# Performance work log

Measured on AMD Instinct MI355X. Metric: run time of the kernel, lower is better.

The kernel has to match this reference:

```python
import jax, jax.numpy as jnp
import numpy as np

SCALE, K, PATCH, STRIDE = 2, 5, 3, 1
EPS = 1e-5


def im2patch(x, p, s):
    # x: (b,c,H,W) -> (b,c,p,p,m1,m2), 'VALID' patches (padding is 0 for our sizes)
    b, c, H, W = x.shape
    m1 = (H - p) // s + 1
    m2 = (W - p) // s + 1
    ii = (jnp.arange(m1) * s)[:, None] + jnp.arange(p)[None, :]   # (m1,p)
    jj = (jnp.arange(m2) * s)[:, None] + jnp.arange(p)[None, :]   # (m2,p)
    pt = x[:, :, ii[:, :, None, None], jj[None, None, :, :]]      # (b,c,m1,p,m2,p)
    return pt.transpose(0, 1, 3, 5, 2, 4)                         # (b,c,p,p,m1,m2)


def patch2im(patches, p, s):
    # overlap-add fold, averaged by per-pixel patch counts (torch F.fold / ones-fold divisor)
    b, c, _, _, m1, m2 = patches.shape
    Hp = (m1 - 1) * s + p
    Wp = (m2 - 1) * s + p
    out = jnp.zeros((b, c, Hp, Wp), patches.dtype)
    cnt = jnp.zeros((Hp, Wp), patches.dtype)
    for i in range(p):          # fixed small loop over patch offsets (p*p = 36)
        for j in range(p):
            out = out.at[:, :, i:i + s * m1:s, j:j + s * m2:s].add(patches[:, :, i, j])
            cnt = cnt.at[i:i + s * m1:s, j:j + s * m2:s].add(1.0)
    return out / cnt


def setup_inputs():
    key = jax.random.key(0)
    k1, k2, k3 = jax.random.split(key, 3)
    b, cy, H, W = 1, 64, 80, 80
    y = jax.random.normal(k1, (b, cy, H, W), jnp.float32)
    yd = jax.random.normal(k2, (b, cy * SCALE ** 2, H // SCALE, W // SCALE), jnp.float32)
    m = ((H - PATCH) // STRIDE + 1) ** 2
    n = ((H // SCALE - PATCH) // STRIDE + 1) ** 2
    idx_k = jax.random.randint(k3, (b, m, K), 0, n, jnp.int32)
    return {"y": y, "yd": yd, "idx_k": idx_k}


def reference(y, yd, idx_k):
    b, cy, H, W = y.shape
    c = yd.shape[1]           # = cy * scale^2
    rs = SCALE ** 2
    y_p = im2patch(y, PATCH, STRIDE)      # (b,cy,p,p,m1,m2)
    yd_p = im2patch(yd, PATCH, STRIDE)    # (b,c,p,p,n1,n2)
    m1, m2 = y_p.shape[-2:]
    n1, n2 = yd_p.shape[-2:]
    m, n = m1 * m2, n1 * n2
    f = c * PATCH * PATCH
    y_flat = y_p.transpose(0, 4, 5, 1, 2, 3).reshape(b, m, f // rs)
    yd_flat = yd_p.transpose(0, 4, 5, 1, 2, 3).reshape(b, n, f)
    # top-k neighbor gather: (b,n,f)[idx (b,m,k)] -> (b,m,k,f) -> (b,m,f,k)
    z = jax.vmap(lambda t, i: t[i])(yd_flat, idx_k)
    z = z.transpose(0, 1, 3, 2)
    # AdaIN: normalize gathered HR patches, apply LR query patch stats (unbiased var, torch default)
    y_n = y_flat.reshape(b, m, c // rs, PATCH * PATCH)
    z_n = z.reshape(b, m, c // rs, rs * PATCH * PATCH, K)
    z_mu = z_n.mean(axis=3, keepdims=True)
    z_sd = jnp.sqrt(z_n.var(axis=3, ddof=1, keepdims=True) + EPS)
    y_mu = y_n.mean(axis=3, keepdims=True)[..., None]        # (b,m,c',1,1)
    y_sd = jnp.sqrt(y_n.var(axis=3, ddof=1, keepdims=True) + EPS)[..., None]
    z = ((z_n - z_mu) / z_sd * y_sd + y_mu).reshape(b, m, f, K)
    # rearrange f = (cy, scale, scale, p1, p2) into SR patches (b, k*cy, p*scale, p*scale, m1, m2)
    z = z.transpose(0, 3, 2, 1)                                   # (b,k,f,m)
    z = z.reshape(b, K, cy, SCALE, SCALE, PATCH, PATCH, m1, m2)
    z = z.transpose(0, 1, 2, 5, 3, 6, 4, 7, 8)                    # (b,k,cy,p1,s,p2,s,m1,m2)
    z = z.reshape(b, K * cy, PATCH * SCALE, PATCH * SCALE, m1, m2)
    z_sr = patch2im(z, PATCH * SCALE, STRIDE * SCALE)             # (b,k*cy,H*scale,W*scale)
    return z_sr.reshape(b, K * cy, H * SCALE, W * SCALE)
```

## Files before the change

kernel.cpp:

```cpp
#include <hip/hip_runtime.h>

#define CY     64
#define HY     80
#define HD     40
#define SPD    (HD*HD)
#define M1     78
#define N1     38
#define M_TOT  (M1*M1)
#define N_TOT  (N1*N1)
#define KK     5
#define HS     160
#define EPSF   1e-5f
#define LP     33

__device__ __forceinline__ unsigned bf16pk(float a, float b) {
    unsigned ua = __float_as_uint(a), ub = __float_as_uint(b);
    ua = (ua + 0x7fffu + ((ua >> 16) & 1u)) >> 16;
    ub = (ub + 0x7fffu + ((ub >> 16) & 1u)) >> 16;
    return ua | (ub << 16);
}

__global__ __launch_bounds__(256) void pre_kernel(const float* __restrict__ y,
                                                  const float* __restrict__ yd,
                                                  uint2* __restrict__ ydT4h,
                                                  float2* __restrict__ zstT,
                                                  float2* __restrict__ ystT) {
    int id = blockIdx.x * 256 + threadIdx.x;
    if (id < SPD * 64) {
        int cc = id & 63, sp = id >> 6;
        float v0 = yd[(cc * 4 + 0) * SPD + sp];
        float v1 = yd[(cc * 4 + 1) * SPD + sp];
        float v2 = yd[(cc * 4 + 2) * SPD + sp];
        float v3 = yd[(cc * 4 + 3) * SPD + sp];
        ydT4h[sp * 64 + cc] = make_uint2(bf16pk(v0, v1), bf16pk(v2, v3));
        return;
    }
    id -= SPD * 64;
    if (id < N_TOT * 64) {
        int n  = id % N_TOT;
        int cc = id / N_TOT;
        int ni = n / N1, nj = n - ni * N1;
        const float* base = yd + (cc * 4) * SPD + ni * HD + nj;
        float s = 0.f, sq = 0.f;
#pragma unroll
        for (int r = 0; r < 4; ++r)
#pragma unroll
            for (int i = 0; i < 3; ++i)
#pragma unroll
                for (int j = 0; j < 3; ++j) {
                    float v = base[r * SPD + i * HD + j];
                    s += v; sq += v * v;
                }
        float mu  = s * (1.f / 36.f);
        float var = (sq - 36.f * mu * mu) * (1.f / 35.f);
        zstT[n * 64 + cc] = make_float2(mu, rsqrtf(var + EPSF));
        return;
    }
    id -= N_TOT * 64;
    if (id >= CY * M_TOT) return;
    int m  = id % M_TOT;
    int cc = id / M_TOT;
    int mi = m / M1, mj = m - mi * M1;
    const float* base = y + cc * (HY * HY) + mi * HY + mj;
    float s = 0.f, sq = 0.f;
#pragma unroll
    for (int i = 0; i < 3; ++i)
#pragma unroll
        for (int j = 0; j < 3; ++j) {
            float v = base[i * HY + j];
            s += v; sq += v * v;
        }
    float mu  = s * (1.f / 9.f);
    float var = (sq - 9.f * mu * mu) * (1.f / 8.f);
    ystT[m * 64 + cc] = make_float2(mu, sqrtf(var + EPSF));
}

__global__ __launch_bounds__(256) void coef_kernel(const int* __restrict__ idx,
                                                   const float2* __restrict__ zstT,
                                                   const float2* __restrict__ ystT,
                                                   unsigned* __restrict__ coef,
                                                   int* __restrict__ nsp) {
    int gid = blockIdx.x * 256 + threadIdx.x;
    int cc = gid & 63;
    int pair = gid >> 6;
    int k = pair / M_TOT, m = pair - k * M_TOT;
    int n = __builtin_amdgcn_readfirstlane(idx[m * KK + k]);
    float2 ys = ystT[m * 64 + cc];
    float2 zs = zstT[n * 64 + cc];
    float a = ys.y * zs.y;
    float b = fmaf(-zs.x, a, ys.x);
    coef[(size_t)pair * 64 + cc] = bf16pk(a, b);
    if (cc == 0) nsp[pair] = (n / N1) * HD + (n - (n / N1) * N1);
}

__device__ __forceinline__ float bflo(unsigned u) { return __uint_as_float(u << 16); }
__device__ __forceinline__ float bfhi(unsigned u) { return __uint_as_float(u & 0xffff0000u); }

__global__ __launch_bounds__(512) void agg_kernel(
    const uint2* __restrict__ ydT4h, const unsigned* __restrict__ coef,
    const int* __restrict__ nsp, float* __restrict__ out)
{
    __shared__ float lds[128 * LP];

    int lane = threadIdx.x & 63;
    int w    = __builtin_amdgcn_readfirstlane(threadIdx.x >> 6);
    int bid  = blockIdx.x;
    int wg   = (bid & 7) * 250 + (bid >> 3);
    int k    = wg / 400;
    int rem  = wg - k * 400;
    int y    = rem / 5;
    int xb2  = rem - y * 5;
    int x0   = xb2 * 16 + w * 2;

    const unsigned* cfk  = coef + (size_t)k * M_TOT * 64;
    const int*      nspk = nsp + k * M_TOT;

    float acc[2][4];
    float bs[2] = {0.f, 0.f};
    float inv[2];
#pragma unroll
    for (int q = 0; q < 2; ++q)
#pragma unroll
        for (int r = 0; r < 4; ++r) acc[q][r] = 0.f;

    if (y >= 2 && y <= M1 - 1 && x0 >= 2 && x0 <= M1 - 2) {
        inv[0] = inv[1] = 1.f / 9.f;
        int      spv[12];
        unsigned cf[12];
#pragma unroll
        for (int p = 0; p < 12; ++p) {
            int m = (y - 2 + (p >> 2)) * M1 + (x0 - 2 + (p & 3));
            spv[p] = nspk[m];
            cf[p]  = cfk[m * 64 + lane];
        }
        int spb[12];
#pragma unroll
        for (int p = 0; p < 12; ++p)
            spb[p] = __builtin_amdgcn_readfirstlane(spv[p]);
#pragma unroll
        for (int r = 0; r < 3; ++r) {
            int b0 = spb[r * 4 + 0] + (2 - r) * HD;
            int b1 = spb[r * 4 + 1] + (2 - r) * HD;
            int b2 = spb[r * 4 + 2] + (2 - r) * HD;
            int b3 = spb[r * 4 + 3] + (2 - r) * HD;
            uint2 vA0 = ydT4h[(b0 + 2) * 64 + lane];
            uint2 vA1 = ydT4h[(b1 + 1) * 64 + lane];
            uint2 vA2 = ydT4h[(b2 + 0) * 64 + lane];
            uint2 vB0 = ydT4h[(b1 + 2) * 64 + lane];
            uint2 vB1 = ydT4h[(b2 + 1) * 64 + lane];
            uint2 vB2 = ydT4h[(b3 + 0) * 64 + lane];
            uint2 vA[3] = {vA0, vA1, vA2};
            uint2 vB[3] = {vB0, vB1, vB2};
#pragma unroll
            for (int c = 0; c < 3; ++c) {
                {
                    unsigned cv = cf[r * 4 + c];
                    float a = bfhi(cv) , dummy;
                    (void)dummy;
                    float aa = bflo(cv), bb = bfhi(cv);
                    bs[0] += bb;
                    acc[0][0] = fmaf(aa, bflo(vA[c].x), acc[0][0]);
                    acc[0][1] = fmaf(aa, bfhi(vA[c].x), acc[0][1]);
                    acc[0][2] = fmaf(aa, bflo(vA[c].y), acc[0][2]);
                    acc[0][3] = fmaf(aa, bfhi(vA[c].y), acc[0][3]);
                    (void)a;
                }
                {
                    unsigned cv = cf[r * 4 + c + 1];
                    float aa = bflo(cv), bb = bfhi(cv);
                    bs[1] += bb;
                    acc[1][0] = fmaf(aa, bflo(vB[c].x), acc[1][0]);
                    acc[1][1] = fmaf(aa, bfhi(vB[c].x), acc[1][1]);
                    acc[1][2] = fmaf(aa, bflo(vB[c].y), acc[1][2]);
                    acc[1][3] = fmaf(aa, bfhi(vB[c].y), acc[1][3]);
                }
            }
        }
    } else {
#pragma unroll
        for (int q = 0; q < 2; ++q) {
            int x = x0 + q;
            int milo = max(0, y - 2), mihi = min(M1 - 1, y);
            int mjlo = max(0, x - 2), mjhi = min(M1 - 1, x);
            inv[q] = 1.f / (float)((mihi - milo + 1) * (mjhi - mjlo + 1));
            for (int mi = milo; mi <= mihi; ++mi)
                for (int mj = mjlo; mj <= mjhi; ++mj) {
                    int m = mi * M1 + mj;
                    unsigned cv = cfk[m * 64 + lane];
                    int sp = __builtin_amdgcn_readfirstlane(nspk[m])
                           + (y - mi) * HD + (x - mj);
                    uint2 vq = ydT4h[sp * 64 + lane];
                    float aa = bflo(cv), bb = bfhi(cv);
                    bs[q] += bb;
                    acc[q][0] = fmaf(aa, bflo(vq.x), acc[q][0]);
                    acc[q][1] = fmaf(aa, bfhi(vq.x), acc[q][1]);
                    acc[q][2] = fmaf(aa, bflo(vq.y), acc[q][2]);
                    acc[q][3] = fmaf(aa, bfhi(vq.y), acc[q][3]);
                }
        }
    }

#pragma unroll
    for (int dy = 0; dy < 2; ++dy)
#pragma unroll
        for (int q = 0; q < 2; ++q) {
            int base = (dy * CY + lane) * LP + (w * 2 + q) * 2;
            lds[base]     = (acc[q][dy * 2]     + bs[q]) * inv[q];
            lds[base + 1] = (acc[q][dy * 2 + 1] + bs[q]) * inv[q];
        }

    __syncthreads();

    int rsel = lane >> 5, c = lane & 31;
    int X0 = xb2 * 32, Y0 = 2 * y;
#pragma unroll
    for (int t = 0; t < 8; ++t) {
        int row = t * 16 + w * 2 + rsel;
        float v = lds[row * LP + c];
        int dy = row >> 6, cc = row & 63;
        out[((size_t)(k * CY + cc) * HS + (Y0 + dy)) * HS + X0 + c] = v;
    }
}

extern "C" void kernel_launch(void* const* d_in, const int* in_sizes, int n_in,
                              void* d_out, int out_size, void* d_ws, size_t ws_size,
                              hipStream_t stream) {
    const float* y   = (const float*)d_in[0];
    const float* yd  = (const float*)d_in[1];
    const int*   idx = (const int*)d_in[2];
    float* out = (float*)d_out;

    char* ws = (char*)d_ws;
    uint2*    ydT4h = (uint2*)ws;
    float2*   zstT  = (float2*)(ws + 819200);
    float2*   ystT  = (float2*)(ws + 819200 + 739328);
    unsigned* coefb = (unsigned*)(ws + 819200 + 739328 + 3115008);
    int*      nspb  = (int*)(ws + 819200 + 739328 + 3115008 + 7787520);

    int pre_total = SPD * 64 + N_TOT * 64 + CY * M_TOT;
    pre_kernel<<<(pre_total + 255) / 256, 256, 0, stream>>>(y, yd, ydT4h, zstT, ystT);
    coef_kernel<<<(KK * M_TOT * 64) / 256, 256, 0, stream>>>(idx, zstT, ystT, coefb, nspb);
    agg_kernel<<<KK * 400, 512, 0, stream>>>(ydT4h, coefb, nspb, out);
}
```

Measured before the change: 37.83 us.

## Switch to fp16 packing with paired-pixel yd layout and packed FMA

The gathered HR data and coefficients now use fp16 instead of bf16. The stats are stored as packed half2. The yd transpose is moved into the coef kernel and stores each pixel together with its right neighbour in a 16-byte entry, so one uint4 load serves two output columns and the interior path needs four loads per row instead of six. Accumulation uses 2-wide vector FMA, and the scalar readfirstlane hints were dropped. The gains are fewer gather loads and possibly packed math, paid for with a doubled yd buffer, fp16 range and precision risk on the stats, and possibly lost scalar addressing.

```diff
diff --git a/kernel.cpp b/kernel.cpp
--- a/kernel.cpp
+++ b/kernel.cpp
@@ -1,4 +1,6 @@
 #include <hip/hip_runtime.h>
+#include <hip/hip_fp16.h>
+#include <string.h>
 
 #define CY     64
 #define HY     80
@@ -13,29 +15,23 @@
 #define EPSF   1e-5f
 #define LP     33
 
-__device__ __forceinline__ unsigned bf16pk(float a, float b) {
-    unsigned ua = __float_as_uint(a), ub = __float_as_uint(b);
-    ua = (ua + 0x7fffu + ((ua >> 16) & 1u)) >> 16;
-    ub = (ub + 0x7fffu + ((ub >> 16) & 1u)) >> 16;
-    return ua | (ub << 16);
-}
-
-__global__ __launch_bounds__(256) void pre_kernel(const float* __restrict__ y,
-                                                  const float* __restrict__ yd,
-                                                  uint2* __restrict__ ydT4h,
-                                                  float2* __restrict__ zstT,
-                                                  float2* __restrict__ ystT) {
+typedef float f32x2 __attribute__((ext_vector_type(2)));
+
+__device__ __forceinline__ unsigned pkf16(float a, float b) {
+    __half2 h = __floats2half2_rn(a, b);
+    unsigned u; memcpy(&u, &h, 4); return u;
+}
+__device__ __forceinline__ f32x2 upk2(unsigned u) {
+    __half2 h; memcpy(&h, &u, 4);
+    float2 f = __half22float2(h);
+    f32x2 r; r.x = f.x; r.y = f.y; return r;
+}
+
+__global__ __launch_bounds__(256) void stats_kernel(const float* __restrict__ y,
+                                                    const float* __restrict__ yd,
+                                                    unsigned* __restrict__ zstP,
+                                                    unsigned* __restrict__ ystP) {
     int id = blockIdx.x * 256 + threadIdx.x;
-    if (id < SPD * 64) {
-        int cc = id & 63, sp = id >> 6;
-        float v0 = yd[(cc * 4 + 0) * SPD + sp];
-        float v1 = yd[(cc * 4 + 1) * SPD + sp];
-        float v2 = yd[(cc * 4 + 2) * SPD + sp];
-        float v3 = yd[(cc * 4 + 3) * SPD + sp];
-        ydT4h[sp * 64 + cc] = make_uint2(bf16pk(v0, v1), bf16pk(v2, v3));
-        return;
-    }
-    id -= SPD * 64;
     if (id < N_TOT * 64) {
         int n  = id % N_TOT;
         int cc = id / N_TOT;
@@ -53,7 +49,7 @@
                 }
         float mu  = s * (1.f / 36.f);
         float var = (sq - 36.f * mu * mu) * (1.f / 35.f);
-        zstT[n * 64 + cc] = make_float2(mu, rsqrtf(var + EPSF));
+        zstP[n * 64 + cc] = pkf16(mu, rsqrtf(var + EPSF));
         return;
     }
     id -= N_TOT * 64;
@@ -72,32 +68,39 @@
         }
     float mu  = s * (1.f / 9.f);
     float var = (sq - 9.f * mu * mu) * (1.f / 8.f);
-    ystT[m * 64 + cc] = make_float2(mu, sqrtf(var + EPSF));
-}
-
-__global__ __launch_bounds__(256) void coef_kernel(const int* __restrict__ idx,
-                                                   const float2* __restrict__ zstT,
-                                                   const float2* __restrict__ ystT,
-                                                   unsigned* __restrict__ coef,
-                                                   int* __restrict__ nsp) {
+    ystP[m * 64 + cc] = pkf16(mu, sqrtf(var + EPSF));
+}
+
+__global__ __launch_bounds__(256) void coef_kernel(const float* __restrict__ yd,
+        const int* __restrict__ idx, const unsigned* __restrict__ zstP,
+        const unsigned* __restrict__ ystP, unsigned* __restrict__ coefP,
+        int* __restrict__ nsp, uint4* __restrict__ ydW) {
     int gid = blockIdx.x * 256 + threadIdx.x;
-    int cc = gid & 63;
-    int pair = gid >> 6;
-    int k = pair / M_TOT, m = pair - k * M_TOT;
-    int n = __builtin_amdgcn_readfirstlane(idx[m * KK + k]);
-    float2 ys = ystT[m * 64 + cc];
-    float2 zs = zstT[n * 64 + cc];
-    float a = ys.y * zs.y;
-    float b = fmaf(-zs.x, a, ys.x);
-    coef[(size_t)pair * 64 + cc] = bf16pk(a, b);
-    if (cc == 0) nsp[pair] = (n / N1) * HD + (n - (n / N1) * N1);
-}
-
-__device__ __forceinline__ float bflo(unsigned u) { return __uint_as_float(u << 16); }
-__device__ __forceinline__ float bfhi(unsigned u) { return __uint_as_float(u & 0xffff0000u); }
+    if (gid < KK * M_TOT * 64) {
+        int cc   = gid & 63;
+        int pair = gid >> 6;
+        int k = pair / M_TOT, m = pair - k * M_TOT;
+        int n = idx[m * KK + k];
+        f32x2 ys = upk2(ystP[m * 64 + cc]);
+        f32x2 zs = upk2(zstP[n * 64 + cc]);
+        float a = ys.y * zs.y;
+        float b = fmaf(-zs.x, a, ys.x);
+        coefP[(size_t)pair * 64 + cc] = pkf16(a, b);
+        if (cc == 0) { int ni = n / N1; nsp[pair] = ni * HD + (n - ni * N1); }
+        return;
+    }
+    gid -= KK * M_TOT * 64;
+    int sp = gid % SPD, cc = gid / SPD;
+    const float* b0 = yd + (cc * 4) * SPD + sp;
+    int d = (sp < SPD - 1) ? 1 : 0;
+    float a0 = b0[0],       a1 = b0[SPD],     a2 = b0[2*SPD],   a3 = b0[3*SPD];
+    float c0 = b0[d],       c1 = b0[SPD+d],   c2 = b0[2*SPD+d], c3 = b0[3*SPD+d];
+    ydW[sp * 64 + cc] = make_uint4(pkf16(a0, a1), pkf16(a2, a3),
+                                   pkf16(c0, c1), pkf16(c2, c3));
+}
 
 __global__ __launch_bounds__(512) void agg_kernel(
-    const uint2* __restrict__ ydT4h, const unsigned* __restrict__ coef,
+    const uint4* __restrict__ ydW, const unsigned* __restrict__ coefP,
     const int* __restrict__ nsp, float* __restrict__ out)
 {
     __shared__ float lds[128 * LP];
@@ -112,69 +115,53 @@
     int xb2  = rem - y * 5;
     int x0   = xb2 * 16 + w * 2;
 
-    const unsigned* cfk  = coef + (size_t)k * M_TOT * 64;
+    const unsigned* cfk  = coefP + (size_t)k * M_TOT * 64;
     const int*      nspk = nsp + k * M_TOT;
 
-    float acc[2][4];
+    f32x2 acc01[2] = {{0.f,0.f},{0.f,0.f}};
+    f32x2 acc23[2] = {{0.f,0.f},{0.f,0.f}};
     float bs[2] = {0.f, 0.f};
-    float inv[2];
-#pragma unroll
-    for (int q = 0; q < 2; ++q)
-#pragma unroll
-        for (int r = 0; r < 4; ++r) acc[q][r] = 0.f;
+    float inv0, inv1;
+
+    auto serve = [&](f32x2& a01, f32x2& a23, float& bsum,
+                     unsigned lo, unsigned hi, float a, float b) {
+        f32x2 am; am.x = a; am.y = a;
+        a01 = __builtin_elementwise_fma(am, upk2(lo), a01);
+        a23 = __builtin_elementwise_fma(am, upk2(hi), a23);
+        bsum += b;
+    };
 
     if (y >= 2 && y <= M1 - 1 && x0 >= 2 && x0 <= M1 - 2) {
-        inv[0] = inv[1] = 1.f / 9.f;
-        int      spv[12];
-        unsigned cf[12];
+        inv0 = inv1 = 1.f / 9.f;
+        unsigned cfu[12];
+        int spb[12];
 #pragma unroll
         for (int p = 0; p < 12; ++p) {
             int m = (y - 2 + (p >> 2)) * M1 + (x0 - 2 + (p & 3));
-            spv[p] = nspk[m];
-            cf[p]  = cfk[m * 64 + lane];
-        }
-        int spb[12];
-#pragma unroll
-        for (int p = 0; p < 12; ++p)
-            spb[p] = __builtin_amdgcn_readfirstlane(spv[p]);
+            cfu[p] = cfk[m * 64 + lane];
+            spb[p] = nspk[m];
+        }
+        float aa[12], bb[12];
+#pragma unroll
+        for (int p = 0; p < 12; ++p) {
+            f32x2 c = upk2(cfu[p]);
+            aa[p] = c.x; bb[p] = c.y;
+        }
 #pragma unroll
         for (int r = 0; r < 3; ++r) {
-            int b0 = spb[r * 4 + 0] + (2 - r) * HD;
-            int b1 = spb[r * 4 + 1] + (2 - r) * HD;
-            int b2 = spb[r * 4 + 2] + (2 - r) * HD;
-            int b3 = spb[r * 4 + 3] + (2 - r) * HD;
-            uint2 vA0 = ydT4h[(b0 + 2) * 64 + lane];
-            uint2 vA1 = ydT4h[(b1 + 1) * 64 + lane];
-            uint2 vA2 = ydT4h[(b2 + 0) * 64 + lane];
-            uint2 vB0 = ydT4h[(b1 + 2) * 64 + lane];
-            uint2 vB1 = ydT4h[(b2 + 1) * 64 + lane];
-            uint2 vB2 = ydT4h[(b3 + 0) * 64 + lane];
-            uint2 vA[3] = {vA0, vA1, vA2};
-            uint2 vB[3] = {vB0, vB1, vB2};
-#pragma unroll
-            for (int c = 0; c < 3; ++c) {
-                {
-                    unsigned cv = cf[r * 4 + c];
-                    float a = bfhi(cv) , dummy;
-                    (void)dummy;
-                    float aa = bflo(cv), bb = bfhi(cv);
-                    bs[0] += bb;
-                    acc[0][0] = fmaf(aa, bflo(vA[c].x), acc[0][0]);
-                    acc[0][1] = fmaf(aa, bfhi(vA[c].x), acc[0][1]);
-                    acc[0][2] = fmaf(aa, bflo(vA[c].y), acc[0][2]);
-                    acc[0][3] = fmaf(aa, bfhi(vA[c].y), acc[0][3]);
-                    (void)a;
-                }
-                {
-                    unsigned cv = cf[r * 4 + c + 1];
-                    float aa = bflo(cv), bb = bfhi(cv);
-                    bs[1] += bb;
-                    acc[1][0] = fmaf(aa, bflo(vB[c].x), acc[1][0]);
-                    acc[1][1] = fmaf(aa, bfhi(vB[c].x), acc[1][1]);
-                    acc[1][2] = fmaf(aa, bflo(vB[c].y), acc[1][2]);
-                    acc[1][3] = fmaf(aa, bfhi(vB[c].y), acc[1][3]);
-                }
-            }
+            int roff = (2 - r) * HD;
+            int s0 = spb[r*4+0] + roff, s1 = spb[r*4+1] + roff;
+            int s2 = spb[r*4+2] + roff, s3 = spb[r*4+3] + roff;
+            uint2 v0 = *(const uint2*)(ydW + (s0 + 2) * 64 + lane);
+            uint4 v1 = ydW[(s1 + 1) * 64 + lane];
+            uint4 v2 = ydW[(s2 + 0) * 64 + lane];
+            uint2 v3 = *(const uint2*)(ydW + (s3 + 0) * 64 + lane);
+            serve(acc01[0], acc23[0], bs[0], v0.x, v0.y, aa[r*4+0], bb[r*4+0]);
+            serve(acc01[0], acc23[0], bs[0], v1.x, v1.y, aa[r*4+1], bb[r*4+1]);
+            serve(acc01[1], acc23[1], bs[1], v1.z, v1.w, aa[r*4+1], bb[r*4+1]);
+            serve(acc01[0], acc23[0], bs[0], v2.x, v2.y, aa[r*4+2], bb[r*4+2]);
+            serve(acc01[1], acc23[1], bs[1], v2.z, v2.w, aa[r*4+2], bb[r*4+2]);
+            serve(acc01[1], acc23[1], bs[1], v3.x, v3.y, aa[r*4+3], bb[r*4+3]);
         }
     } else {
 #pragma unroll
@@ -182,32 +169,30 @@
             int x = x0 + q;
             int milo = max(0, y - 2), mihi = min(M1 - 1, y);
             int mjlo = max(0, x - 2), mjhi = min(M1 - 1, x);
-            inv[q] = 1.f / (float)((mihi - milo + 1) * (mjhi - mjlo + 1));
+            float iv = 1.f / (float)((mihi - milo + 1) * (mjhi - mjlo + 1));
+            if (q == 0) inv0 = iv; else inv1 = iv;
             for (int mi = milo; mi <= mihi; ++mi)
                 for (int mj = mjlo; mj <= mjhi; ++mj) {
                     int m = mi * M1 + mj;
-                    unsigned cv = cfk[m * 64 + lane];
-                    int sp = __builtin_amdgcn_readfirstlane(nspk[m])
-                           + (y - mi) * HD + (x - mj);
-                    uint2 vq = ydT4h[sp * 64 + lane];
-                    float aa = bflo(cv), bb = bfhi(cv);
-                    bs[q] += bb;
-                    acc[q][0] = fmaf(aa, bflo(vq.x), acc[q][0]);
-                    acc[q][1] = fmaf(aa, bfhi(vq.x), acc[q][1]);
-                    acc[q][2] = fmaf(aa, bflo(vq.y), acc[q][2]);
-                    acc[q][3] = fmaf(aa, bfhi(vq.y), acc[q][3]);
+                    f32x2 c = upk2(cfk[m * 64 + lane]);
+                    int sp = nspk[m] + (y - mi) * HD + (x - mj);
+                    uint2 v = *(const uint2*)(ydW + sp * 64 + lane);
+                    if (q == 0) serve(acc01[0], acc23[0], bs[0], v.x, v.y, c.x, c.y);
+                    else        serve(acc01[1], acc23[1], bs[1], v.x, v.y, c.x, c.y);
                 }
         }
     }
 
 #pragma unroll
-    for (int dy = 0; dy < 2; ++dy)
-#pragma unroll
-        for (int q = 0; q < 2; ++q) {
-            int base = (dy * CY + lane) * LP + (w * 2 + q) * 2;
-            lds[base]     = (acc[q][dy * 2]     + bs[q]) * inv[q];
-            lds[base + 1] = (acc[q][dy * 2 + 1] + bs[q]) * inv[q];
-        }
+    for (int q = 0; q < 2; ++q) {
+        float iv = q ? inv1 : inv0;
+        float bq = bs[q];
+        int col = (w * 2 + q) * 2;
+        lds[(0 * CY + lane) * LP + col]     = (acc01[q].x + bq) * iv;
+        lds[(0 * CY + lane) * LP + col + 1] = (acc01[q].y + bq) * iv;
+        lds[(1 * CY + lane) * LP + col]     = (acc23[q].x + bq) * iv;
+        lds[(1 * CY + lane) * LP + col + 1] = (acc23[q].y + bq) * iv;
+    }
 
     __syncthreads();
 
@@ -231,14 +216,16 @@
     float* out = (float*)d_out;
 
     char* ws = (char*)d_ws;
-    uint2*    ydT4h = (uint2*)ws;
-    float2*   zstT  = (float2*)(ws + 819200);
-    float2*   ystT  = (float2*)(ws + 819200 + 739328);
-    unsigned* coefb = (unsigned*)(ws + 819200 + 739328 + 3115008);
-    int*      nspb  = (int*)(ws + 819200 + 739328 + 3115008 + 7787520);
-
-    int pre_total = SPD * 64 + N_TOT * 64 + CY * M_TOT;
-    pre_kernel<<<(pre_total + 255) / 256, 256, 0, stream>>>(y, yd, ydT4h, zstT, ystT);
-    coef_kernel<<<(KK * M_TOT * 64) / 256, 256, 0, stream>>>(idx, zstT, ystT, coefb, nspb);
-    agg_kernel<<<KK * 400, 512, 0, stream>>>(ydT4h, coefb, nspb, out);
-}
+    uint4*    ydW   = (uint4*)ws;
+    unsigned* zstP  = (unsigned*)(ws + 1638400);
+    unsigned* ystP  = (unsigned*)(ws + 2008064);
+    unsigned* coefP = (unsigned*)(ws + 3565568);
+    int*      nspb  = (int*)(ws + 11353088);
+
+    int stats_total = N_TOT * 64 + CY * M_TOT;
+    stats_kernel<<<(stats_total + 255) / 256, 256, 0, stream>>>(y, yd, zstP, ystP);
+    int coef_total = KK * M_TOT * 64 + SPD * 64;
+    coef_kernel<<<(coef_total + 255) / 256, 256, 0, stream>>>(yd, idx, zstP, ystP,
+                                                              coefP, nspb, ydW);
+    agg_kernel<<<KK * 400, 512, 0, stream>>>(ydW, coefP, nspb, out);
+}
```

After: 38.35 us. About the same (+1.4%).
